# Kernel optimization log

Hardware: AMD Instinct MI355X
Metric: run time of the kernel (lower is better)

The kernel has to match this reference:

```python
import jax, jax.numpy as jnp
import numpy as np

EPS_NORM = 1e-12  # F.normalize eps
BN_EPS = 1e-5     # BatchNorm2d eps
N_NODES = 18
T_STEPS = 1280
FC_IN = 1469952


def _temporal_conv(x, wa, ba, wb, bb, wc, bc):
    """Gated temporal conv (GLU) from STConv's TemporalConv.
    x: (B, T, N, C) -> (B, T-k+1, N, Cout)."""
    xp = jnp.transpose(x, (0, 3, 2, 1))  # (B, C, N, T)

    def conv(w, b):
        y = jax.lax.conv_general_dilated(
            xp, w, window_strides=(1, 1), padding='VALID',
            dimension_numbers=('NCHW', 'OIHW', 'NCHW'))
        return y + b[None, :, None, None]

    P = conv(wa, ba)
    Q = jax.nn.sigmoid(conv(wb, bb))
    H = jax.nn.relu(P * Q + conv(wc, bc))
    return jnp.transpose(H, (0, 3, 2, 1))  # (B, T', N, Cout)


def setup_inputs() -> dict:
    key = jax.random.key(0)
    ks = jax.random.split(key, 16)
    s = 0.05
    inp = {
        'x': jax.random.normal(ks[0], (N_NODES, 1, T_STEPS), dtype=jnp.float32),
        'edge_index': jax.random.randint(ks[1], (2, 306), 0, N_NODES, dtype=jnp.int64),
        'edge_weight': jax.random.uniform(ks[2], (306,), dtype=jnp.float32),
        'w1a': jax.random.normal(ks[3], (64, 1, 1, 3), dtype=jnp.float32) * s,
        'b1a': jnp.zeros((64,), jnp.float32),
        'w1b': jax.random.normal(ks[4], (64, 1, 1, 3), dtype=jnp.float32) * s,
        'b1b': jnp.zeros((64,), jnp.float32),
        'w1c': jax.random.normal(ks[5], (64, 1, 1, 3), dtype=jnp.float32) * s,
        'b1c': jnp.zeros((64,), jnp.float32),
        'cheb_w': jax.random.normal(ks[6], (64, 64), dtype=jnp.float32) * s,
        'cheb_b': jnp.zeros((64,), jnp.float32),
        'w2a': jax.random.normal(ks[7], (64, 64, 1, 3), dtype=jnp.float32) * s,
        'b2a': jnp.zeros((64,), jnp.float32),
        'w2b': jax.random.normal(ks[8], (64, 64, 1, 3), dtype=jnp.float32) * s,
        'b2b': jnp.zeros((64,), jnp.float32),
        'w2c': jax.random.normal(ks[9], (64, 64, 1, 3), dtype=jnp.float32) * s,
        'b2c': jnp.zeros((64,), jnp.float32),
        'bn_gamma': jnp.ones((N_NODES,), jnp.float32),
        'bn_beta': jnp.zeros((N_NODES,), jnp.float32),
        'fc_w': jax.random.normal(ks[10], (1, FC_IN), dtype=jnp.float32) * 0.001,
        'fc_b': jnp.zeros((1,), jnp.float32),
    }
    return inp


def reference(x, edge_index, edge_weight,
              w1a, b1a, w1b, b1b, w1c, b1c,
              cheb_w, cheb_b,
              w2a, b2a, w2b, b2b, w2c, b2c,
              bn_gamma, bn_beta, fc_w, fc_b):
    # F.normalize(x, dim=1): x shape (N, 1, T)
    norm = jnp.sqrt(jnp.sum(x * x, axis=1, keepdims=True))
    xn = x / jnp.maximum(norm, EPS_NORM)
    # x[None].reshape([1, shape[3], shape[1], shape[2]]): row-major reshape (faithful)
    X = jnp.reshape(xn[None], (1, xn.shape[2], xn.shape[0], xn.shape[1]))  # (1, T, N, 1)

    T0 = _temporal_conv(X, w1a, b1a, w1b, b1b, w1c, b1c)  # (1, T-2, N, 64)
    # ChebConv with K=1: only T_0 = I term -> per-node linear; edge_index/edge_weight unused
    T = jnp.einsum('btnc,cd->btnd', T0, cheb_w) + cheb_b
    T = jax.nn.relu(T)
    T = _temporal_conv(T, w2a, b2a, w2b, b2b, w2c, b2c)  # (1, T-4, N, 64)

    # BatchNorm2d(num_nodes) in training mode: normalize per-node over (B, T, C)
    Tp = jnp.transpose(T, (0, 2, 1, 3))  # (B, N, T, C)
    mean = jnp.mean(Tp, axis=(0, 2, 3), keepdims=True)
    var = jnp.mean((Tp - mean) ** 2, axis=(0, 2, 3), keepdims=True)  # biased var
    Tn = (Tp - mean) / jnp.sqrt(var + BN_EPS)
    Tn = Tn * bn_gamma[None, :, None, None] + bn_beta[None, :, None, None]
    h = jnp.transpose(Tn, (0, 2, 1, 3))  # (B, T-4, N, C)

    h = jax.nn.relu(h).reshape(-1)  # flatten(start_dim=0)
    return fc_w @ h + fc_b  # (1,)
```

## Files before the change

kernel.cpp:

```cpp
#include <hip/hip_runtime.h>
#include <math.h>

#define NN 18
#define T_STEPS 1280
#define T1LEN 1278
#define T2LEN 1276
#define NPOS1 (T1LEN * NN)
#define XTOT  (T_STEPS * NN)
#define PC1 32
#define NCHUNK1 ((NPOS1 + PC1 - 1) / PC1)
#define PREPBLK 144
#define TC2 64
#define NCHUNK2 ((T2LEN + TC2 - 1) / TC2)
#define NBLK (NCHUNK2 * NN)

typedef __attribute__((ext_vector_type(8))) short short8;
typedef __attribute__((ext_vector_type(4))) float f32x4;

__device__ __forceinline__ unsigned short f2bf(float v) {
    unsigned u = __builtin_bit_cast(unsigned, v);
    u = u + 0x7fff + ((u >> 16) & 1);
    return (unsigned short)(u >> 16);
}
__device__ __forceinline__ float bf2f(unsigned short h) {
    unsigned u = ((unsigned)h) << 16;
    return __builtin_bit_cast(float, u);
}

__global__ __launch_bounds__(256) void k_fused1x(const float* __restrict__ x,
        const float* __restrict__ w1a, const float* __restrict__ b1a,
        const float* __restrict__ w1b, const float* __restrict__ b1b,
        const float* __restrict__ w1c, const float* __restrict__ b1c,
        const float* __restrict__ cw, const float* __restrict__ cb,
        const float* __restrict__ w2a, const float* __restrict__ w2b,
        const float* __restrict__ w2c,
        unsigned short* __restrict__ T1hi, unsigned short* __restrict__ T1lo,
        unsigned short* __restrict__ WBhi, unsigned short* __restrict__ WBlo) {
    int b = blockIdx.x;
    int tid = threadIdx.x;
    if (b >= NCHUNK1) {
        int i = (b - NCHUNK1) * 256 + tid;
        int klocal = i & 31;
        int col = (i >> 5) % 192;
        int kb = i / (192 * 32);
        int conv = col >> 6, co = col & 63;
        int k = kb >> 1, ci = (kb & 1) * 32 + klocal;
        const float* w = (conv == 0) ? w2a : (conv == 1 ? w2b : w2c);
        float v = w[co * 192 + ci * 3 + k];
        unsigned short hi = f2bf(v);
        WBhi[i] = hi;
        WBlo[i] = f2bf(v - bf2f(hi));
        return;
    }
    __shared__ float xs[72];
    __shared__ uint4 tileH4[256], tileL4[256];
    unsigned short* tileH = (unsigned short*)tileH4;
    unsigned short* tileL = (unsigned short*)tileL4;
    int p0 = b * PC1;
    int np = min(PC1, NPOS1 - p0);
    for (int idx = tid; idx < PC1 + 36; idx += 256) {
        int g = p0 + idx;
        float v = (g < XTOT) ? x[g] : 0.f;
        xs[idx] = v / fmaxf(fabsf(v), 1e-12f);
    }
    __syncthreads();
    int l = tid & 63, w = tid >> 6;
    int c = l;
    {
        float wa0 = w1a[c*3], wa1 = w1a[c*3+1], wa2 = w1a[c*3+2];
        float wb0 = w1b[c*3], wb1 = w1b[c*3+1], wb2 = w1b[c*3+2];
        float wc0 = w1c[c*3], wc1 = w1c[c*3+1], wc2 = w1c[c*3+2];
        float ba = b1a[c], bb = b1b[c], bc = b1c[c];
        #pragma unroll
        for (int j = 0; j < 8; ++j) {
            int pl = w * 8 + j;
            float x0 = xs[pl], x1 = xs[pl + 18], x2 = xs[pl + 36];
            float pa = fmaf(wa2, x2, fmaf(wa1, x1, fmaf(wa0, x0, ba)));
            float pb = fmaf(wb2, x2, fmaf(wb1, x1, fmaf(wb0, x0, bb)));
            float pc_ = fmaf(wc2, x2, fmaf(wc1, x1, fmaf(wc0, x0, bc)));
            float q = 1.0f / (1.0f + expf(-pb));
            float v = fmaxf(pa * q + pc_, 0.f);
            unsigned short hi = f2bf(v);
            int sw = pl * 64 + (((c >> 3) ^ (pl & 7)) << 3) + (c & 7);
            tileH[sw] = hi;
            tileL[sw] = f2bf(v - bf2f(hi));
        }
    }
    int d = w * 16 + (l & 15);
    short8 cbh[2], cbl[2];
    #pragma unroll
    for (int kb = 0; kb < 2; ++kb) {
        #pragma unroll
        for (int j = 0; j < 8; ++j) {
            float v = cw[(kb * 32 + (l >> 4) * 8 + j) * 64 + d];
            unsigned short hi = f2bf(v);
            cbh[kb][j] = (short)hi;
            cbl[kb][j] = (short)f2bf(v - bf2f(hi));
        }
    }
    __syncthreads();
    f32x4 acc[2] = {{0.f,0.f,0.f,0.f},{0.f,0.f,0.f,0.f}};
    #pragma unroll
    for (int kb = 0; kb < 2; ++kb) {
        #pragma unroll
        for (int mt = 0; mt < 2; ++mt) {
            int row = mt * 16 + (l & 15);
            int cbi = kb * 4 + (l >> 4);
            int si = row * 8 + (cbi ^ (row & 7));
            short8 ah = __builtin_bit_cast(short8, tileH4[si]);
            short8 al = __builtin_bit_cast(short8, tileL4[si]);
            acc[mt] = __builtin_amdgcn_mfma_f32_16x16x32_bf16(ah, cbh[kb], acc[mt], 0, 0, 0);
            acc[mt] = __builtin_amdgcn_mfma_f32_16x16x32_bf16(al, cbh[kb], acc[mt], 0, 0, 0);
            acc[mt] = __builtin_amdgcn_mfma_f32_16x16x32_bf16(ah, cbl[kb], acc[mt], 0, 0, 0);
        }
    }
    float cbias = cb[d];
    #pragma unroll
    for (int mt = 0; mt < 2; ++mt) {
        #pragma unroll
        for (int r = 0; r < 4; ++r) {
            int p = mt * 16 + (l >> 4) * 4 + r;
            if (p < np) {
                float v = fmaxf(acc[mt][r] + cbias, 0.f);
                unsigned short hi = f2bf(v);
                int idx = (p0 + p) * 64 + d;
                T1hi[idx] = hi;
                T1lo[idx] = f2bf(v - bf2f(hi));
            }
        }
    }
}

__device__ __forceinline__ void conv2_compute(
        const unsigned short* __restrict__ T1hi, const unsigned short* __restrict__ T1lo,
        const unsigned short* __restrict__ WBhi, const unsigned short* __restrict__ WBlo,
        const float* __restrict__ b2a, const float* __restrict__ b2b,
        const float* __restrict__ b2c,
        uint4* ldsH, uint4* ldsL,
        int node, int t0, int tid, float h[16], float* s_sum, float* s_sq) {
    int rows_valid = min(66, T1LEN - t0);
    const uint4* gh = (const uint4*)T1hi;
    const uint4* gl = (const uint4*)T1lo;
    for (int idx = tid; idx < 528; idx += 256) {
        int row = idx >> 3, cb2 = idx & 7;
        uint4 vh = {0,0,0,0}, vl = {0,0,0,0};
        if (row < rows_valid) {
            int g = ((t0 + row) * NN + node) * 8 + cb2;
            vh = gh[g]; vl = gl[g];
        }
        int s = row * 8 + (cb2 ^ (row & 7));
        ldsH[s] = vh; ldsL[s] = vl;
    }
    int l = tid & 63, w = tid >> 6;
    int co = w * 16 + (l & 15);
    __syncthreads();
    const uint4* wbh = (const uint4*)WBhi;
    const uint4* wbl = (const uint4*)WBlo;
    f32x4 acc[4][3];
    #pragma unroll
    for (int mt = 0; mt < 4; ++mt)
        #pragma unroll
        for (int ct = 0; ct < 3; ++ct)
            acc[mt][ct] = (f32x4){0.f, 0.f, 0.f, 0.f};
    for (int kb = 0; kb < 6; ++kb) {
        short8 bh[3], bl[3];
        #pragma unroll
        for (int ct = 0; ct < 3; ++ct) {
            int col = (w + 4 * ct) * 16 + (l & 15);
            int gi = (kb * 192 + col) * 4 + (l >> 4);
            bh[ct] = __builtin_bit_cast(short8, wbh[gi]);
            bl[ct] = __builtin_bit_cast(short8, wbl[gi]);
        }
        #pragma unroll
        for (int mt = 0; mt < 4; ++mt) {
            int row = mt * 16 + (l & 15) + (kb >> 1);
            int cb2 = (kb & 1) * 4 + (l >> 4);
            int si = row * 8 + (cb2 ^ (row & 7));
            short8 ah = __builtin_bit_cast(short8, ldsH[si]);
            short8 al = __builtin_bit_cast(short8, ldsL[si]);
            acc[mt][0] = __builtin_amdgcn_mfma_f32_16x16x32_bf16(ah, bh[0], acc[mt][0], 0, 0, 0);
            acc[mt][1] = __builtin_amdgcn_mfma_f32_16x16x32_bf16(ah, bh[1], acc[mt][1], 0, 0, 0);
            acc[mt][2] = __builtin_amdgcn_mfma_f32_16x16x32_bf16(ah, bh[2], acc[mt][2], 0, 0, 0);
            acc[mt][0] = __builtin_amdgcn_mfma_f32_16x16x32_bf16(al, bh[0], acc[mt][0], 0, 0, 0);
            acc[mt][1] = __builtin_amdgcn_mfma_f32_16x16x32_bf16(al, bh[1], acc[mt][1], 0, 0, 0);
            acc[mt][2] = __builtin_amdgcn_mfma_f32_16x16x32_bf16(al, bh[2], acc[mt][2], 0, 0, 0);
            acc[mt][0] = __builtin_amdgcn_mfma_f32_16x16x32_bf16(ah, bl[0], acc[mt][0], 0, 0, 0);
            acc[mt][1] = __builtin_amdgcn_mfma_f32_16x16x32_bf16(ah, bl[1], acc[mt][1], 0, 0, 0);
            acc[mt][2] = __builtin_amdgcn_mfma_f32_16x16x32_bf16(ah, bl[2], acc[mt][2], 0, 0, 0);
        }
    }
    float ba = b2a[co], bb = b2b[co], bc = b2c[co];
    float ssum = 0.f, ssq = 0.f;
    #pragma unroll
    for (int mt = 0; mt < 4; ++mt) {
        #pragma unroll
        for (int r = 0; r < 4; ++r) {
            int t = t0 + mt * 16 + (l >> 4) * 4 + r;
            float hv = 0.f;
            if (t < T2LEN) {
                float P = acc[mt][0][r] + ba, Q = acc[mt][1][r] + bb, Cc = acc[mt][2][r] + bc;
                float qs = 1.f / (1.f + expf(-Q));
                hv = fmaxf(fmaf(P, qs, Cc), 0.f);
                ssum += hv;
                ssq = fmaf(hv, hv, ssq);
            }
            h[mt * 4 + r] = hv;
        }
    }
    *s_sum = ssum; *s_sq = ssq;
}

__global__ __launch_bounds__(256) void k_conv2s(
        const unsigned short* __restrict__ T1hi, const unsigned short* __restrict__ T1lo,
        const unsigned short* __restrict__ WBhi, const unsigned short* __restrict__ WBlo,
        const float* __restrict__ b2a, const float* __restrict__ b2b,
        const float* __restrict__ b2c, float* __restrict__ partials) {
    __shared__ uint4 ldsH[528], ldsL[528];
    __shared__ float rs[256], rq[256];
    int b = blockIdx.x;
    int node = b / NCHUNK2, chunk = b % NCHUNK2;
    int t0 = chunk * TC2;
    int tid = threadIdx.x;
    float h[16], s_sum, s_sq;
    conv2_compute(T1hi, T1lo, WBhi, WBlo, b2a, b2b, b2c, ldsH, ldsL,
                  node, t0, tid, h, &s_sum, &s_sq);
    rs[tid] = s_sum; rq[tid] = s_sq;
    __syncthreads();
    for (int off = 128; off > 0; off >>= 1) {
        if (tid < off) { rs[tid] += rs[tid + off]; rq[tid] += rq[tid + off]; }
        __syncthreads();
    }
    if (tid == 0) {
        partials[b * 2]     = rs[0];
        partials[b * 2 + 1] = rq[0];
    }
}

__global__ __launch_bounds__(256) void k_dotbn(
        const unsigned short* __restrict__ T1hi, const unsigned short* __restrict__ T1lo,
        const unsigned short* __restrict__ WBhi, const unsigned short* __restrict__ WBlo,
        const float* __restrict__ b2a, const float* __restrict__ b2b,
        const float* __restrict__ b2c,
        const float* __restrict__ partials,
        const float* __restrict__ gamma, const float* __restrict__ beta,
        const float* __restrict__ fcw, float* __restrict__ dpart) {
    __shared__ uint4 ldsH[528], ldsL[528];
    __shared__ float rr[256];
    int b = blockIdx.x;
    int node = b / NCHUNK2, chunk = b % NCHUNK2;
    int t0 = chunk * TC2;
    int tid = threadIdx.x;
    float h[16], s_sum, s_sq;
    conv2_compute(T1hi, T1lo, WBhi, WBlo, b2a, b2b, b2c, ldsH, ldsL,
                  node, t0, tid, h, &s_sum, &s_sq);
    float s = 0.f, q = 0.f;
    #pragma unroll
    for (int i = 0; i < NCHUNK2; ++i) {
        s += partials[(node * NCHUNK2 + i) * 2];
        q += partials[(node * NCHUNK2 + i) * 2 + 1];
    }
    float cnt = (float)(T2LEN * 64);
    float mean = s / cnt;
    float var = q / cnt - mean * mean;
    float istd = rsqrtf(var + 1e-5f);
    float g = gamma[node], bt = beta[node];
    int l = tid & 63, w = tid >> 6;
    int co = w * 16 + (l & 15);
    float acc = 0.f;
    #pragma unroll
    for (int mt = 0; mt < 4; ++mt) {
        #pragma unroll
        for (int r = 0; r < 4; ++r) {
            int t = t0 + mt * 16 + (l >> 4) * 4 + r;
            if (t < T2LEN) {
                float v = fmaxf((h[mt * 4 + r] - mean) * istd * g + bt, 0.f);
                acc = fmaf(v, fcw[(t * NN + node) * 64 + co], acc);
            }
        }
    }
    rr[tid] = acc;
    __syncthreads();
    for (int off = 128; off > 0; off >>= 1) {
        if (tid < off) rr[tid] += rr[tid + off];
        __syncthreads();
    }
    if (tid == 0) dpart[b] = rr[0];
}

__global__ __launch_bounds__(256) void k_final(const float* __restrict__ dpart,
                                               const float* __restrict__ fcb,
                                               float* __restrict__ out) {
    __shared__ float r[256];
    float v = 0.f;
    for (int i = threadIdx.x; i < NBLK; i += 256) v += dpart[i];
    r[threadIdx.x] = v;
    __syncthreads();
    for (int off = 128; off > 0; off >>= 1) {
        if (threadIdx.x < off) r[threadIdx.x] += r[threadIdx.x + off];
        __syncthreads();
    }
    if (threadIdx.x == 0) out[0] = r[0] + fcb[0];
}

extern "C" void kernel_launch(void* const* d_in, const int* in_sizes, int n_in,
                              void* d_out, int out_size, void* d_ws, size_t ws_size,
                              hipStream_t stream) {
    const float* x     = (const float*)d_in[0];
    const float* w1a   = (const float*)d_in[3];
    const float* b1a   = (const float*)d_in[4];
    const float* w1b   = (const float*)d_in[5];
    const float* b1b   = (const float*)d_in[6];
    const float* w1c   = (const float*)d_in[7];
    const float* b1c   = (const float*)d_in[8];
    const float* chw   = (const float*)d_in[9];
    const float* chb   = (const float*)d_in[10];
    const float* w2a   = (const float*)d_in[11];
    const float* b2a   = (const float*)d_in[12];
    const float* w2b   = (const float*)d_in[13];
    const float* b2b   = (const float*)d_in[14];
    const float* w2c   = (const float*)d_in[15];
    const float* b2c   = (const float*)d_in[16];
    const float* gamma = (const float*)d_in[17];
    const float* beta  = (const float*)d_in[18];
    const float* fcw   = (const float*)d_in[19];
    const float* fcb   = (const float*)d_in[20];
    float* out = (float*)d_out;

    char* base = (char*)d_ws;
    unsigned short* T1hi  = (unsigned short*)(base);
    unsigned short* T1lo  = (unsigned short*)(base + 2944512);
    unsigned short* WBhi  = (unsigned short*)(base + 5889024);
    unsigned short* WBlo  = (unsigned short*)(base + 5962752);
    float*          parts = (float*)(base + 6036480);
    float*          dpart = (float*)(base + 6039360);

    k_fused1x<<<NCHUNK1 + PREPBLK, 256, 0, stream>>>(
        x, w1a, b1a, w1b, b1b, w1c, b1c, chw, chb,
        w2a, w2b, w2c, T1hi, T1lo, WBhi, WBlo);
    k_conv2s<<<NBLK, 256, 0, stream>>>(
        T1hi, T1lo, WBhi, WBlo, b2a, b2b, b2c, parts);
    k_dotbn<<<NBLK, 256, 0, stream>>>(
        T1hi, T1lo, WBhi, WBlo, b2a, b2b, b2c, parts, gamma, beta, fcw, dpart);
    k_final<<<1, 256, 0, stream>>>(dpart, fcb, out);
}
```

Measured before the change: 33.54 us.

## Fuse conv2 stats, BN-dot and final reduce into one kernel with grid barrier

Merges the conv2 statistics pass, the BN+FC dot pass and the final reduction into a single kernel. Blocks publish per-block sum and sum-of-squares, then spin on an atomic counter as a grid-wide barrier. The conv2 computation now runs once instead of twice, and two launches are dropped. The last block to finish does the final reduction, selected with a second atomic counter. The spin barrier assumes all 360 blocks are co-resident (launch_bounds 256,2 is meant to help), so the cost is deadlock risk and spin overhead.

New measurement: 66.84 us. 1.99x slower.

```diff
diff --git a/kernel.cpp b/kernel.cpp
--- a/kernel.cpp
+++ b/kernel.cpp
@@ -35,11 +35,13 @@
         const float* __restrict__ w2a, const float* __restrict__ w2b,
         const float* __restrict__ w2c,
         unsigned short* __restrict__ T1hi, unsigned short* __restrict__ T1lo,
-        unsigned short* __restrict__ WBhi, unsigned short* __restrict__ WBlo) {
+        unsigned short* __restrict__ WBhi, unsigned short* __restrict__ WBlo,
+        int* __restrict__ cnt1, int* __restrict__ cnt2) {
     int b = blockIdx.x;
     int tid = threadIdx.x;
     if (b >= NCHUNK1) {
         int i = (b - NCHUNK1) * 256 + tid;
+        if (i == 0) { *cnt1 = 0; *cnt2 = 0; }
         int klocal = i & 31;
         int col = (i >> 5) % 192;
         int kb = i / (192 * 32);
@@ -210,13 +212,19 @@
     *s_sum = ssum; *s_sq = ssq;
 }
 
-__global__ __launch_bounds__(256) void k_conv2s(
+__global__ __launch_bounds__(256, 2) void k_conv2dot(
         const unsigned short* __restrict__ T1hi, const unsigned short* __restrict__ T1lo,
         const unsigned short* __restrict__ WBhi, const unsigned short* __restrict__ WBlo,
         const float* __restrict__ b2a, const float* __restrict__ b2b,
-        const float* __restrict__ b2c, float* __restrict__ partials) {
+        const float* __restrict__ b2c,
+        const float* __restrict__ gamma, const float* __restrict__ beta,
+        const float* __restrict__ fcw, const float* __restrict__ fcb,
+        float* parts, float* dpart, int* cnt1, int* cnt2,
+        float* __restrict__ out) {
     __shared__ uint4 ldsH[528], ldsL[528];
-    __shared__ float rs[256], rq[256];
+    __shared__ float red1[256], red2[256];
+    __shared__ float pl[2 * NCHUNK2];
+    __shared__ int lastFlag;
     int b = blockIdx.x;
     int node = b / NCHUNK2, chunk = b % NCHUNK2;
     int t0 = chunk * TC2;
@@ -224,44 +232,31 @@
     float h[16], s_sum, s_sq;
     conv2_compute(T1hi, T1lo, WBhi, WBlo, b2a, b2b, b2c, ldsH, ldsL,
                   node, t0, tid, h, &s_sum, &s_sq);
-    rs[tid] = s_sum; rq[tid] = s_sq;
+    red1[tid] = s_sum; red2[tid] = s_sq;
     __syncthreads();
     for (int off = 128; off > 0; off >>= 1) {
-        if (tid < off) { rs[tid] += rs[tid + off]; rq[tid] += rq[tid + off]; }
+        if (tid < off) { red1[tid] += red1[tid + off]; red2[tid] += red2[tid + off]; }
         __syncthreads();
     }
     if (tid == 0) {
-        partials[b * 2]     = rs[0];
-        partials[b * 2 + 1] = rq[0];
-    }
-}
-
-__global__ __launch_bounds__(256) void k_dotbn(
-        const unsigned short* __restrict__ T1hi, const unsigned short* __restrict__ T1lo,
-        const unsigned short* __restrict__ WBhi, const unsigned short* __restrict__ WBlo,
-        const float* __restrict__ b2a, const float* __restrict__ b2b,
-        const float* __restrict__ b2c,
-        const float* __restrict__ partials,
-        const float* __restrict__ gamma, const float* __restrict__ beta,
-        const float* __restrict__ fcw, float* __restrict__ dpart) {
-    __shared__ uint4 ldsH[528], ldsL[528];
-    __shared__ float rr[256];
-    int b = blockIdx.x;
-    int node = b / NCHUNK2, chunk = b % NCHUNK2;
-    int t0 = chunk * TC2;
-    int tid = threadIdx.x;
-    float h[16], s_sum, s_sq;
-    conv2_compute(T1hi, T1lo, WBhi, WBlo, b2a, b2b, b2c, ldsH, ldsL,
-                  node, t0, tid, h, &s_sum, &s_sq);
+        __hip_atomic_store(&parts[b * 2],     red1[0], __ATOMIC_RELEASE, __HIP_MEMORY_SCOPE_AGENT);
+        __hip_atomic_store(&parts[b * 2 + 1], red2[0], __ATOMIC_RELEASE, __HIP_MEMORY_SCOPE_AGENT);
+        __threadfence();
+        atomicAdd(cnt1, 1);
+        while (__hip_atomic_load(cnt1, __ATOMIC_ACQUIRE, __HIP_MEMORY_SCOPE_AGENT) < NBLK)
+            __builtin_amdgcn_s_sleep(2);
+    }
+    __syncthreads();
+    if (tid < 2 * NCHUNK2)
+        pl[tid] = __hip_atomic_load(&parts[node * 2 * NCHUNK2 + tid],
+                                    __ATOMIC_ACQUIRE, __HIP_MEMORY_SCOPE_AGENT);
+    __syncthreads();
     float s = 0.f, q = 0.f;
     #pragma unroll
-    for (int i = 0; i < NCHUNK2; ++i) {
-        s += partials[(node * NCHUNK2 + i) * 2];
-        q += partials[(node * NCHUNK2 + i) * 2 + 1];
-    }
-    float cnt = (float)(T2LEN * 64);
-    float mean = s / cnt;
-    float var = q / cnt - mean * mean;
+    for (int i = 0; i < NCHUNK2; ++i) { s += pl[2 * i]; q += pl[2 * i + 1]; }
+    float cntf = (float)(T2LEN * 64);
+    float mean = s / cntf;
+    float var = q / cntf - mean * mean;
     float istd = rsqrtf(var + 1e-5f);
     float g = gamma[node], bt = beta[node];
     int l = tid & 63, w = tid >> 6;
@@ -278,28 +273,31 @@
             }
         }
     }
-    rr[tid] = acc;
+    red1[tid] = acc;
     __syncthreads();
     for (int off = 128; off > 0; off >>= 1) {
-        if (tid < off) rr[tid] += rr[tid + off];
+        if (tid < off) red1[tid] += red1[tid + off];
         __syncthreads();
     }
-    if (tid == 0) dpart[b] = rr[0];
-}
-
-__global__ __launch_bounds__(256) void k_final(const float* __restrict__ dpart,
-                                               const float* __restrict__ fcb,
-                                               float* __restrict__ out) {
-    __shared__ float r[256];
-    float v = 0.f;
-    for (int i = threadIdx.x; i < NBLK; i += 256) v += dpart[i];
-    r[threadIdx.x] = v;
-    __syncthreads();
-    for (int off = 128; off > 0; off >>= 1) {
-        if (threadIdx.x < off) r[threadIdx.x] += r[threadIdx.x + off];
+    if (tid == 0) {
+        __hip_atomic_store(&dpart[b], red1[0], __ATOMIC_RELEASE, __HIP_MEMORY_SCOPE_AGENT);
+        __threadfence();
+        int old = atomicAdd(cnt2, 1);
+        lastFlag = (old == NBLK - 1);
+    }
+    __syncthreads();
+    if (lastFlag) {
+        float v = 0.f;
+        for (int i = tid; i < NBLK; i += 256)
+            v += __hip_atomic_load(&dpart[i], __ATOMIC_ACQUIRE, __HIP_MEMORY_SCOPE_AGENT);
+        red1[tid] = v;
         __syncthreads();
-    }
-    if (threadIdx.x == 0) out[0] = r[0] + fcb[0];
+        for (int off = 128; off > 0; off >>= 1) {
+            if (tid < off) red1[tid] += red1[tid + off];
+            __syncthreads();
+        }
+        if (tid == 0) out[0] = red1[0] + fcb[0];
+    }
 }
 
 extern "C" void kernel_launch(void* const* d_in, const int* in_sizes, int n_in,
@@ -333,13 +331,13 @@
     unsigned short* WBlo  = (unsigned short*)(base + 5962752);
     float*          parts = (float*)(base + 6036480);
     float*          dpart = (float*)(base + 6039360);
+    int*            cnt1  = (int*)(base + 6040800);
+    int*            cnt2  = (int*)(base + 6040804);
 
     k_fused1x<<<NCHUNK1 + PREPBLK, 256, 0, stream>>>(
         x, w1a, b1a, w1b, b1b, w1c, b1c, chw, chb,
-        w2a, w2b, w2c, T1hi, T1lo, WBhi, WBlo);
-    k_conv2s<<<NBLK, 256, 0, stream>>>(
-        T1hi, T1lo, WBhi, WBlo, b2a, b2b, b2c, parts);
-    k_dotbn<<<NBLK, 256, 0, stream>>>(
-        T1hi, T1lo, WBhi, WBlo, b2a, b2b, b2c, parts, gamma, beta, fcw, dpart);
-    k_final<<<1, 256, 0, stream>>>(dpart, fcb, out);
-}
+        w2a, w2b, w2c, T1hi, T1lo, WBhi, WBlo, cnt1, cnt2);
+    k_conv2dot<<<NBLK, 256, 0, stream>>>(
+        T1hi, T1lo, WBhi, WBlo, b2a, b2b, b2c,
+        gamma, beta, fcw, fcb, parts, dpart, cnt1, cnt2, out);
+}
```

## Fuse conv1, Cheb and conv2 per node-chunk; store T2 once; stream BN+FC dot

Applied to the files above, without the earlier changes.

Stage 1 (temporal conv + Cheb linear) is now computed per node/time chunk directly into LDS and fed to conv2 in the same block, so the bf16 hi/lo T1 intermediate no longer goes through global memory. Conv2 also runs only once: its fp32 output is written to global, and a separate grid-stride kernel applies BatchNorm, ReLU and the FC dot with float4 loads. Before, conv2 was recomputed a second time to avoid storing it. The chunk size drops to 62 so that the 2-row halo fits in a 64-row tile, which means stage 1 is recomputed on the overlapping rows. In exchange the code writes and reads a 5.9MB fp32 T2 buffer and adds a separate weight-prep launch.

Result: faster. 30.87 us (-8.0%).

```diff
diff --git a/kernel.cpp b/kernel.cpp
--- a/kernel.cpp
+++ b/kernel.cpp
@@ -5,14 +5,11 @@
 #define T_STEPS 1280
 #define T1LEN 1278
 #define T2LEN 1276
-#define NPOS1 (T1LEN * NN)
-#define XTOT  (T_STEPS * NN)
-#define PC1 32
-#define NCHUNK1 ((NPOS1 + PC1 - 1) / PC1)
 #define PREPBLK 144
-#define TC2 64
+#define TC2 62
 #define NCHUNK2 ((T2LEN + TC2 - 1) / TC2)
 #define NBLK (NCHUNK2 * NN)
+#define DOT_BLOCKS 512
 
 typedef __attribute__((ext_vector_type(8))) short short8;
 typedef __attribute__((ext_vector_type(4))) float f32x4;
@@ -26,64 +23,75 @@
     unsigned u = ((unsigned)h) << 16;
     return __builtin_bit_cast(float, u);
 }
-
-__global__ __launch_bounds__(256) void k_fused1x(const float* __restrict__ x,
+__device__ __forceinline__ int swz(int row, int c) {
+    return row * 64 + (((c >> 3) ^ (row & 7)) << 3) + (c & 7);
+}
+
+__global__ void k_wprep(const float* __restrict__ wa, const float* __restrict__ wb,
+                        const float* __restrict__ wc,
+                        unsigned short* __restrict__ WBhi, unsigned short* __restrict__ WBlo) {
+    int i = blockIdx.x * 256 + threadIdx.x;
+    if (i >= 6 * 192 * 32) return;
+    int klocal = i & 31;
+    int col = (i >> 5) % 192;
+    int kb = i / (192 * 32);
+    int conv = col >> 6, co = col & 63;
+    int k = kb >> 1, ci = (kb & 1) * 32 + klocal;
+    const float* w = (conv == 0) ? wa : (conv == 1 ? wb : wc);
+    float v = w[co * 192 + ci * 3 + k];
+    unsigned short hi = f2bf(v);
+    WBhi[i] = hi;
+    WBlo[i] = f2bf(v - bf2f(hi));
+}
+
+__global__ __launch_bounds__(256) void k_fuseall(const float* __restrict__ x,
         const float* __restrict__ w1a, const float* __restrict__ b1a,
         const float* __restrict__ w1b, const float* __restrict__ b1b,
         const float* __restrict__ w1c, const float* __restrict__ b1c,
         const float* __restrict__ cw, const float* __restrict__ cb,
-        const float* __restrict__ w2a, const float* __restrict__ w2b,
-        const float* __restrict__ w2c,
-        unsigned short* __restrict__ T1hi, unsigned short* __restrict__ T1lo,
-        unsigned short* __restrict__ WBhi, unsigned short* __restrict__ WBlo) {
+        const unsigned short* __restrict__ WBhi, const unsigned short* __restrict__ WBlo,
+        const float* __restrict__ b2a, const float* __restrict__ b2b,
+        const float* __restrict__ b2c,
+        float* __restrict__ T2, float* __restrict__ parts) {
+    __shared__ float xs[66];
+    __shared__ uint4 t1H[512], t1L[512];
+    __shared__ uint4 t2H[528], t2L[528];
+    __shared__ float red1[256], red2[256];
     int b = blockIdx.x;
+    int node = b / NCHUNK2, chunk = b % NCHUNK2;
+    int t0 = chunk * TC2;
     int tid = threadIdx.x;
-    if (b >= NCHUNK1) {
-        int i = (b - NCHUNK1) * 256 + tid;
-        int klocal = i & 31;
-        int col = (i >> 5) % 192;
-        int kb = i / (192 * 32);
-        int conv = col >> 6, co = col & 63;
-        int k = kb >> 1, ci = (kb & 1) * 32 + klocal;
-        const float* w = (conv == 0) ? w2a : (conv == 1 ? w2b : w2c);
-        float v = w[co * 192 + ci * 3 + k];
-        unsigned short hi = f2bf(v);
-        WBhi[i] = hi;
-        WBlo[i] = f2bf(v - bf2f(hi));
-        return;
-    }
-    __shared__ float xs[72];
-    __shared__ uint4 tileH4[256], tileL4[256];
-    unsigned short* tileH = (unsigned short*)tileH4;
-    unsigned short* tileL = (unsigned short*)tileL4;
-    int p0 = b * PC1;
-    int np = min(PC1, NPOS1 - p0);
-    for (int idx = tid; idx < PC1 + 36; idx += 256) {
-        int g = p0 + idx;
-        float v = (g < XTOT) ? x[g] : 0.f;
-        xs[idx] = v / fmaxf(fabsf(v), 1e-12f);
-    }
-    __syncthreads();
     int l = tid & 63, w = tid >> 6;
-    int c = l;
+
+    if (tid < 66) {
+        int xt = t0 + tid;
+        float v = (xt < T_STEPS) ? x[xt * NN + node] : 0.f;
+        xs[tid] = v / fmaxf(fabsf(v), 1e-12f);
+    }
+    __syncthreads();
+
     {
+        unsigned short* tH = (unsigned short*)t1H;
+        unsigned short* tL = (unsigned short*)t1L;
+        int c = l;
         float wa0 = w1a[c*3], wa1 = w1a[c*3+1], wa2 = w1a[c*3+2];
         float wb0 = w1b[c*3], wb1 = w1b[c*3+1], wb2 = w1b[c*3+2];
         float wc0 = w1c[c*3], wc1 = w1c[c*3+1], wc2 = w1c[c*3+2];
         float ba = b1a[c], bb = b1b[c], bc = b1c[c];
         #pragma unroll
-        for (int j = 0; j < 8; ++j) {
-            int pl = w * 8 + j;
-            float x0 = xs[pl], x1 = xs[pl + 18], x2 = xs[pl + 36];
+        for (int j = 0; j < 16; ++j) {
+            int r = w * 16 + j;
+            float x0 = xs[r], x1 = xs[r + 1], x2 = xs[r + 2];
             float pa = fmaf(wa2, x2, fmaf(wa1, x1, fmaf(wa0, x0, ba)));
             float pb = fmaf(wb2, x2, fmaf(wb1, x1, fmaf(wb0, x0, bb)));
             float pc_ = fmaf(wc2, x2, fmaf(wc1, x1, fmaf(wc0, x0, bc)));
             float q = 1.0f / (1.0f + expf(-pb));
             float v = fmaxf(pa * q + pc_, 0.f);
+            if (t0 + r >= T1LEN) v = 0.f;
             unsigned short hi = f2bf(v);
-            int sw = pl * 64 + (((c >> 3) ^ (pl & 7)) << 3) + (c & 7);
-            tileH[sw] = hi;
-            tileL[sw] = f2bf(v - bf2f(hi));
+            int sw = swz(r, c);
+            tH[sw] = hi;
+            tL[sw] = f2bf(v - bf2f(hi));
         }
     }
     int d = w * 16 + (l & 15);
@@ -99,203 +107,171 @@
         }
     }
     __syncthreads();
-    f32x4 acc[2] = {{0.f,0.f,0.f,0.f},{0.f,0.f,0.f,0.f}};
-    #pragma unroll
-    for (int kb = 0; kb < 2; ++kb) {
-        #pragma unroll
-        for (int mt = 0; mt < 2; ++mt) {
-            int row = mt * 16 + (l & 15);
-            int cbi = kb * 4 + (l >> 4);
-            int si = row * 8 + (cbi ^ (row & 7));
-            short8 ah = __builtin_bit_cast(short8, tileH4[si]);
-            short8 al = __builtin_bit_cast(short8, tileL4[si]);
-            acc[mt] = __builtin_amdgcn_mfma_f32_16x16x32_bf16(ah, cbh[kb], acc[mt], 0, 0, 0);
-            acc[mt] = __builtin_amdgcn_mfma_f32_16x16x32_bf16(al, cbh[kb], acc[mt], 0, 0, 0);
-            acc[mt] = __builtin_amdgcn_mfma_f32_16x16x32_bf16(ah, cbl[kb], acc[mt], 0, 0, 0);
-        }
-    }
-    float cbias = cb[d];
-    #pragma unroll
-    for (int mt = 0; mt < 2; ++mt) {
-        #pragma unroll
-        for (int r = 0; r < 4; ++r) {
-            int p = mt * 16 + (l >> 4) * 4 + r;
-            if (p < np) {
+    {
+        f32x4 acc[4];
+        #pragma unroll
+        for (int mt = 0; mt < 4; ++mt) acc[mt] = (f32x4){0.f,0.f,0.f,0.f};
+        #pragma unroll
+        for (int kb = 0; kb < 2; ++kb) {
+            #pragma unroll
+            for (int mt = 0; mt < 4; ++mt) {
+                int row = mt * 16 + (l & 15);
+                int cbi = kb * 4 + (l >> 4);
+                int si = row * 8 + (cbi ^ (row & 7));
+                short8 ah = __builtin_bit_cast(short8, t1H[si]);
+                short8 al = __builtin_bit_cast(short8, t1L[si]);
+                acc[mt] = __builtin_amdgcn_mfma_f32_16x16x32_bf16(ah, cbh[kb], acc[mt], 0, 0, 0);
+                acc[mt] = __builtin_amdgcn_mfma_f32_16x16x32_bf16(al, cbh[kb], acc[mt], 0, 0, 0);
+                acc[mt] = __builtin_amdgcn_mfma_f32_16x16x32_bf16(ah, cbl[kb], acc[mt], 0, 0, 0);
+            }
+        }
+        float cbias = cb[d];
+        unsigned short* tH = (unsigned short*)t2H;
+        unsigned short* tL = (unsigned short*)t2L;
+        #pragma unroll
+        for (int mt = 0; mt < 4; ++mt) {
+            #pragma unroll
+            for (int r = 0; r < 4; ++r) {
+                int row = mt * 16 + (l >> 4) * 4 + r;
                 float v = fmaxf(acc[mt][r] + cbias, 0.f);
+                if (t0 + row >= T1LEN) v = 0.f;
                 unsigned short hi = f2bf(v);
-                int idx = (p0 + p) * 64 + d;
-                T1hi[idx] = hi;
-                T1lo[idx] = f2bf(v - bf2f(hi));
-            }
-        }
-    }
-}
-
-__device__ __forceinline__ void conv2_compute(
-        const unsigned short* __restrict__ T1hi, const unsigned short* __restrict__ T1lo,
-        const unsigned short* __restrict__ WBhi, const unsigned short* __restrict__ WBlo,
-        const float* __restrict__ b2a, const float* __restrict__ b2b,
-        const float* __restrict__ b2c,
-        uint4* ldsH, uint4* ldsL,
-        int node, int t0, int tid, float h[16], float* s_sum, float* s_sq) {
-    int rows_valid = min(66, T1LEN - t0);
-    const uint4* gh = (const uint4*)T1hi;
-    const uint4* gl = (const uint4*)T1lo;
-    for (int idx = tid; idx < 528; idx += 256) {
-        int row = idx >> 3, cb2 = idx & 7;
-        uint4 vh = {0,0,0,0}, vl = {0,0,0,0};
-        if (row < rows_valid) {
-            int g = ((t0 + row) * NN + node) * 8 + cb2;
-            vh = gh[g]; vl = gl[g];
-        }
-        int s = row * 8 + (cb2 ^ (row & 7));
-        ldsH[s] = vh; ldsL[s] = vl;
-    }
-    int l = tid & 63, w = tid >> 6;
-    int co = w * 16 + (l & 15);
-    __syncthreads();
-    const uint4* wbh = (const uint4*)WBhi;
-    const uint4* wbl = (const uint4*)WBlo;
-    f32x4 acc[4][3];
-    #pragma unroll
-    for (int mt = 0; mt < 4; ++mt)
-        #pragma unroll
-        for (int ct = 0; ct < 3; ++ct)
-            acc[mt][ct] = (f32x4){0.f, 0.f, 0.f, 0.f};
-    for (int kb = 0; kb < 6; ++kb) {
-        short8 bh[3], bl[3];
-        #pragma unroll
-        for (int ct = 0; ct < 3; ++ct) {
-            int col = (w + 4 * ct) * 16 + (l & 15);
-            int gi = (kb * 192 + col) * 4 + (l >> 4);
-            bh[ct] = __builtin_bit_cast(short8, wbh[gi]);
-            bl[ct] = __builtin_bit_cast(short8, wbl[gi]);
-        }
+                int sw = swz(row, d);
+                tH[sw] = hi;
+                tL[sw] = f2bf(v - bf2f(hi));
+            }
+        }
+        if (tid < 128) {
+            int row = 64 + (tid >> 6), c = tid & 63;
+            int sw = swz(row, c);
+            tH[sw] = 0; tL[sw] = 0;
+        }
+    }
+    __syncthreads();
+    float s_sum = 0.f, s_sq = 0.f;
+    {
+        const uint4* wbh = (const uint4*)WBhi;
+        const uint4* wbl = (const uint4*)WBlo;
+        int co = w * 16 + (l & 15);
+        f32x4 acc[4][3];
+        #pragma unroll
+        for (int mt = 0; mt < 4; ++mt)
+            #pragma unroll
+            for (int ct = 0; ct < 3; ++ct)
+                acc[mt][ct] = (f32x4){0.f, 0.f, 0.f, 0.f};
+        for (int kb = 0; kb < 6; ++kb) {
+            short8 bh[3], bl[3];
+            #pragma unroll
+            for (int ct = 0; ct < 3; ++ct) {
+                int col = (w + 4 * ct) * 16 + (l & 15);
+                int gi = (kb * 192 + col) * 4 + (l >> 4);
+                bh[ct] = __builtin_bit_cast(short8, wbh[gi]);
+                bl[ct] = __builtin_bit_cast(short8, wbl[gi]);
+            }
+            #pragma unroll
+            for (int mt = 0; mt < 4; ++mt) {
+                int row = mt * 16 + (l & 15) + (kb >> 1);
+                int cb2 = (kb & 1) * 4 + (l >> 4);
+                int si = row * 8 + (cb2 ^ (row & 7));
+                short8 ah = __builtin_bit_cast(short8, t2H[si]);
+                short8 al = __builtin_bit_cast(short8, t2L[si]);
+                acc[mt][0] = __builtin_amdgcn_mfma_f32_16x16x32_bf16(ah, bh[0], acc[mt][0], 0, 0, 0);
+                acc[mt][1] = __builtin_amdgcn_mfma_f32_16x16x32_bf16(ah, bh[1], acc[mt][1], 0, 0, 0);
+                acc[mt][2] = __builtin_amdgcn_mfma_f32_16x16x32_bf16(ah, bh[2], acc[mt][2], 0, 0, 0);
+                acc[mt][0] = __builtin_amdgcn_mfma_f32_16x16x32_bf16(al, bh[0], acc[mt][0], 0, 0, 0);
+                acc[mt][1] = __builtin_amdgcn_mfma_f32_16x16x32_bf16(al, bh[1], acc[mt][1], 0, 0, 0);
+                acc[mt][2] = __builtin_amdgcn_mfma_f32_16x16x32_bf16(al, bh[2], acc[mt][2], 0, 0, 0);
+                acc[mt][0] = __builtin_amdgcn_mfma_f32_16x16x32_bf16(ah, bl[0], acc[mt][0], 0, 0, 0);
+                acc[mt][1] = __builtin_amdgcn_mfma_f32_16x16x32_bf16(ah, bl[1], acc[mt][1], 0, 0, 0);
+                acc[mt][2] = __builtin_amdgcn_mfma_f32_16x16x32_bf16(ah, bl[2], acc[mt][2], 0, 0, 0);
+            }
+        }
+        float ba = b2a[co], bb = b2b[co], bc = b2c[co];
         #pragma unroll
         for (int mt = 0; mt < 4; ++mt) {
-            int row = mt * 16 + (l & 15) + (kb >> 1);
-            int cb2 = (kb & 1) * 4 + (l >> 4);
-            int si = row * 8 + (cb2 ^ (row & 7));
-            short8 ah = __builtin_bit_cast(short8, ldsH[si]);
-            short8 al = __builtin_bit_cast(short8, ldsL[si]);
-            acc[mt][0] = __builtin_amdgcn_mfma_f32_16x16x32_bf16(ah, bh[0], acc[mt][0], 0, 0, 0);
-            acc[mt][1] = __builtin_amdgcn_mfma_f32_16x16x32_bf16(ah, bh[1], acc[mt][1], 0, 0, 0);
-            acc[mt][2] = __builtin_amdgcn_mfma_f32_16x16x32_bf16(ah, bh[2], acc[mt][2], 0, 0, 0);
-            acc[mt][0] = __builtin_amdgcn_mfma_f32_16x16x32_bf16(al, bh[0], acc[mt][0], 0, 0, 0);
-            acc[mt][1] = __builtin_amdgcn_mfma_f32_16x16x32_bf16(al, bh[1], acc[mt][1], 0, 0, 0);
-            acc[mt][2] = __builtin_amdgcn_mfma_f32_16x16x32_bf16(al, bh[2], acc[mt][2], 0, 0, 0);
-            acc[mt][0] = __builtin_amdgcn_mfma_f32_16x16x32_bf16(ah, bl[0], acc[mt][0], 0, 0, 0);
-            acc[mt][1] = __builtin_amdgcn_mfma_f32_16x16x32_bf16(ah, bl[1], acc[mt][1], 0, 0, 0);
-            acc[mt][2] = __builtin_amdgcn_mfma_f32_16x16x32_bf16(ah, bl[2], acc[mt][2], 0, 0, 0);
-        }
-    }
-    float ba = b2a[co], bb = b2b[co], bc = b2c[co];
-    float ssum = 0.f, ssq = 0.f;
-    #pragma unroll
-    for (int mt = 0; mt < 4; ++mt) {
-        #pragma unroll
-        for (int r = 0; r < 4; ++r) {
-            int t = t0 + mt * 16 + (l >> 4) * 4 + r;
-            float hv = 0.f;
-            if (t < T2LEN) {
-                float P = acc[mt][0][r] + ba, Q = acc[mt][1][r] + bb, Cc = acc[mt][2][r] + bc;
-                float qs = 1.f / (1.f + expf(-Q));
-                hv = fmaxf(fmaf(P, qs, Cc), 0.f);
-                ssum += hv;
-                ssq = fmaf(hv, hv, ssq);
-            }
-            h[mt * 4 + r] = hv;
-        }
-    }
-    *s_sum = ssum; *s_sq = ssq;
-}
-
-__global__ __launch_bounds__(256) void k_conv2s(
-        const unsigned short* __restrict__ T1hi, const unsigned short* __restrict__ T1lo,
-        const unsigned short* __restrict__ WBhi, const unsigned short* __restrict__ WBlo,
-        const float* __restrict__ b2a, const float* __restrict__ b2b,
-        const float* __restrict__ b2c, float* __restrict__ partials) {
-    __shared__ uint4 ldsH[528], ldsL[528];
-    __shared__ float rs[256], rq[256];
-    int b = blockIdx.x;
-    int node = b / NCHUNK2, chunk = b % NCHUNK2;
-    int t0 = chunk * TC2;
-    int tid = threadIdx.x;
-    float h[16], s_sum, s_sq;
-    conv2_compute(T1hi, T1lo, WBhi, WBlo, b2a, b2b, b2c, ldsH, ldsL,
-                  node, t0, tid, h, &s_sum, &s_sq);
-    rs[tid] = s_sum; rq[tid] = s_sq;
+            #pragma unroll
+            for (int r = 0; r < 4; ++r) {
+                int tl2 = mt * 16 + (l >> 4) * 4 + r;
+                int t = t0 + tl2;
+                if (tl2 < TC2 && t < T2LEN) {
+                    float P = acc[mt][0][r] + ba, Q = acc[mt][1][r] + bb, Cc = acc[mt][2][r] + bc;
+                    float qs = 1.f / (1.f + expf(-Q));
+                    float hv = fmaxf(fmaf(P, qs, Cc), 0.f);
+                    T2[(t * NN + node) * 64 + co] = hv;
+                    s_sum += hv;
+                    s_sq = fmaf(hv, hv, s_sq);
+                }
+            }
+        }
+    }
+    red1[tid] = s_sum; red2[tid] = s_sq;
     __syncthreads();
     for (int off = 128; off > 0; off >>= 1) {
-        if (tid < off) { rs[tid] += rs[tid + off]; rq[tid] += rq[tid + off]; }
+        if (tid < off) { red1[tid] += red1[tid + off]; red2[tid] += red2[tid + off]; }
         __syncthreads();
     }
     if (tid == 0) {
-        partials[b * 2]     = rs[0];
-        partials[b * 2 + 1] = rq[0];
-    }
-}
-
-__global__ __launch_bounds__(256) void k_dotbn(
-        const unsigned short* __restrict__ T1hi, const unsigned short* __restrict__ T1lo,
-        const unsigned short* __restrict__ WBhi, const unsigned short* __restrict__ WBlo,
-        const float* __restrict__ b2a, const float* __restrict__ b2b,
-        const float* __restrict__ b2c,
-        const float* __restrict__ partials,
+        parts[b * 2]     = red1[0];
+        parts[b * 2 + 1] = red2[0];
+    }
+}
+
+__global__ __launch_bounds__(256) void k_dot2(const float* __restrict__ T2,
+        const float* __restrict__ parts,
         const float* __restrict__ gamma, const float* __restrict__ beta,
         const float* __restrict__ fcw, float* __restrict__ dpart) {
-    __shared__ uint4 ldsH[528], ldsL[528];
-    __shared__ float rr[256];
-    int b = blockIdx.x;
-    int node = b / NCHUNK2, chunk = b % NCHUNK2;
-    int t0 = chunk * TC2;
-    int tid = threadIdx.x;
-    float h[16], s_sum, s_sq;
-    conv2_compute(T1hi, T1lo, WBhi, WBlo, b2a, b2b, b2c, ldsH, ldsL,
-                  node, t0, tid, h, &s_sum, &s_sq);
-    float s = 0.f, q = 0.f;
-    #pragma unroll
-    for (int i = 0; i < NCHUNK2; ++i) {
-        s += partials[(node * NCHUNK2 + i) * 2];
-        q += partials[(node * NCHUNK2 + i) * 2 + 1];
-    }
-    float cnt = (float)(T2LEN * 64);
-    float mean = s / cnt;
-    float var = q / cnt - mean * mean;
-    float istd = rsqrtf(var + 1e-5f);
-    float g = gamma[node], bt = beta[node];
-    int l = tid & 63, w = tid >> 6;
-    int co = w * 16 + (l & 15);
+    __shared__ float sm[NN * 4];
+    if (threadIdx.x < NN) {
+        int n = threadIdx.x;
+        float s = 0.f, q = 0.f;
+        for (int i = 0; i < NCHUNK2; ++i) {
+            s += parts[(n * NCHUNK2 + i) * 2];
+            q += parts[(n * NCHUNK2 + i) * 2 + 1];
+        }
+        float cnt = (float)(T2LEN * 64);
+        float mean = s / cnt;
+        float var = q / cnt - mean * mean;
+        sm[n * 4]     = mean;
+        sm[n * 4 + 1] = rsqrtf(var + 1e-5f);
+        sm[n * 4 + 2] = gamma[n];
+        sm[n * 4 + 3] = beta[n];
+    }
+    __syncthreads();
     float acc = 0.f;
-    #pragma unroll
-    for (int mt = 0; mt < 4; ++mt) {
-        #pragma unroll
-        for (int r = 0; r < 4; ++r) {
-            int t = t0 + mt * 16 + (l >> 4) * 4 + r;
-            if (t < T2LEN) {
-                float v = fmaxf((h[mt * 4 + r] - mean) * istd * g + bt, 0.f);
-                acc = fmaf(v, fcw[(t * NN + node) * 64 + co], acc);
-            }
-        }
-    }
-    rr[tid] = acc;
+    const int total4 = T2LEN * NN * 64 / 4;
+    const float4* T24 = (const float4*)T2;
+    const float4* fw4 = (const float4*)fcw;
+    for (int i = blockIdx.x * 256 + threadIdx.x; i < total4; i += DOT_BLOCKS * 256) {
+        float4 t = T24[i];
+        float4 f = fw4[i];
+        int n = (i >> 4) % NN;
+        float mu = sm[n * 4], is = sm[n * 4 + 1], g = sm[n * 4 + 2], bt = sm[n * 4 + 3];
+        float v0 = fmaxf((t.x - mu) * is * g + bt, 0.f);
+        float v1 = fmaxf((t.y - mu) * is * g + bt, 0.f);
+        float v2 = fmaxf((t.z - mu) * is * g + bt, 0.f);
+        float v3 = fmaxf((t.w - mu) * is * g + bt, 0.f);
+        acc = fmaf(v0, f.x, acc);
+        acc = fmaf(v1, f.y, acc);
+        acc = fmaf(v2, f.z, acc);
+        acc = fmaf(v3, f.w, acc);
+    }
+    __shared__ float r[256];
+    r[threadIdx.x] = acc;
     __syncthreads();
     for (int off = 128; off > 0; off >>= 1) {
-        if (tid < off) rr[tid] += rr[tid + off];
+        if (threadIdx.x < off) r[threadIdx.x] += r[threadIdx.x + off];
         __syncthreads();
     }
-    if (tid == 0) dpart[b] = rr[0];
-}
-
-__global__ __launch_bounds__(256) void k_final(const float* __restrict__ dpart,
+    if (threadIdx.x == 0) dpart[blockIdx.x] = r[0];
+}
+
+__global__ __launch_bounds__(512) void k_final(const float* __restrict__ dpart,
                                                const float* __restrict__ fcb,
                                                float* __restrict__ out) {
-    __shared__ float r[256];
-    float v = 0.f;
-    for (int i = threadIdx.x; i < NBLK; i += 256) v += dpart[i];
-    r[threadIdx.x] = v;
-    __syncthreads();
-    for (int off = 128; off > 0; off >>= 1) {
+    __shared__ float r[512];
+    r[threadIdx.x] = dpart[threadIdx.x];
+    __syncthreads();
+    for (int off = 256; off > 0; off >>= 1) {
         if (threadIdx.x < off) r[threadIdx.x] += r[threadIdx.x + off];
         __syncthreads();
     }
@@ -327,19 +303,16 @@
     float* out = (float*)d_out;
 
     char* base = (char*)d_ws;
-    unsigned short* T1hi  = (unsigned short*)(base);
-    unsigned short* T1lo  = (unsigned short*)(base + 2944512);
-    unsigned short* WBhi  = (unsigned short*)(base + 5889024);
-    unsigned short* WBlo  = (unsigned short*)(base + 5962752);
-    float*          parts = (float*)(base + 6036480);
-    float*          dpart = (float*)(base + 6039360);
-
-    k_fused1x<<<NCHUNK1 + PREPBLK, 256, 0, stream>>>(
+    float*          T2v   = (float*)(base);
+    unsigned short* WBhi  = (unsigned short*)(base + 5879808);
+    unsigned short* WBlo  = (unsigned short*)(base + 5953536);
+    float*          parts = (float*)(base + 6027264);
+    float*          dpart = (float*)(base + 6030336);
+
+    k_wprep<<<PREPBLK, 256, 0, stream>>>(w2a, w2b, w2c, WBhi, WBlo);
+    k_fuseall<<<NBLK, 256, 0, stream>>>(
         x, w1a, b1a, w1b, b1b, w1c, b1c, chw, chb,
-        w2a, w2b, w2c, T1hi, T1lo, WBhi, WBlo);
-    k_conv2s<<<NBLK, 256, 0, stream>>>(
-        T1hi, T1lo, WBhi, WBlo, b2a, b2b, b2c, parts);
-    k_dotbn<<<NBLK, 256, 0, stream>>>(
-        T1hi, T1lo, WBhi, WBlo, b2a, b2b, b2c, parts, gamma, beta, fcw, dpart);
-    k_final<<<1, 256, 0, stream>>>(dpart, fcb, out);
-}
+        WBhi, WBlo, b2a, b2b, b2c, T2v, parts);
+    k_dot2<<<DOT_BLOCKS, 256, 0, stream>>>(T2v, parts, gamma, beta, fcw, dpart);
+    k_final<<<1, 512, 0, stream>>>(dpart, fcb, out);
+}
```
